# Kernel tuning notes

Hardware: AMD Instinct MI355X
Metric: run time of the kernel (lower is better)

Reference implementation:

```python
import jax, jax.numpy as jnp
import numpy as np

# Explicit-duration HSMM forward DP in log space.
# Recursion (all quantities in log space):
#   entry[t, j] = pi[j]                                   if t == 0
#               = logsumexp_i alpha[t-1, i] + A[i, j]      otherwise
#   alpha[t, j] = logsumexp_{d=1..min(Dmax, t+1)}
#                   entry[t-d+1, j] + D[j, d] + sum_{u=t-d+1..t} log_B[u, j]
#   loglik      = logsumexp_j alpha[T-1, j]

NEG = -1.0e30  # finite -inf sentinel (autodiff-safe)
B, T, S, DMAX = 64, 2048, 128, 128


def setup_inputs() -> dict:
    key = jax.random.key(0)
    k1, k2, k3, k4 = jax.random.split(key, 4)
    # emission log-likelihoods per (batch, time, state); need not normalize over states
    log_B = jax.random.normal(k1, (B, T, S), dtype=jnp.float32)
    # normalized log-prob buffers, matching the module's buffer constraints
    pi_logits = jax.nn.log_softmax(jax.random.normal(k2, (S,), dtype=jnp.float32))
    A_raw = jax.random.normal(k3, (S, S), dtype=jnp.float32)
    # SEMI transition constraint: no self-transitions (diagonal ~ -inf), rows normalized
    A_logits = jax.nn.log_softmax(
        jnp.where(jnp.eye(S, dtype=bool), -1.0e9, A_raw), axis=1)
    D_logits = jax.nn.log_softmax(
        jax.random.normal(k4, (S, DMAX), dtype=jnp.float32), axis=1)
    return {"log_B": log_B, "pi_logits": pi_logits,
            "A_logits": A_logits, "D_logits": D_logits}


def _hsmm_forward_loglik(log_B, pi_logits, A_logits, D_logits):
    Bn, Tn, Sn = log_B.shape
    Dm = D_logits.shape[1]
    lb = jnp.transpose(log_B, (1, 0, 2))                         # (T, B, S)
    # cum[k] = sum_{u < k} log_B[u]; front-padded with Dm zero rows (masked anyway)
    cum = jnp.concatenate(
        [jnp.zeros((1, Bn, Sn), lb.dtype), jnp.cumsum(lb, axis=0)], axis=0)
    cum_pad = jnp.concatenate(
        [jnp.zeros((Dm, Bn, Sn), lb.dtype), cum], axis=0)        # (T+Dm+1, B, S)
    logD = D_logits.T[:, None, :]                                # (Dm, 1, S)
    dur = jnp.arange(1, Dm + 1)[:, None, None]                   # (Dm, 1, 1)

    def step(carry, t):
        entry_buf, alpha_prev = carry                            # (Dm,B,S), (B,S)
        # transition into state j after a segment ended at t-1
        trans = jax.nn.logsumexp(
            alpha_prev[:, :, None] + A_logits[None, :, :], axis=1)  # (B, S)
        entry_t = jnp.where(t == 0, pi_logits[None, :], trans)
        # entry_buf[d-1] = entry[t-d+1]
        entry_buf = jnp.roll(entry_buf, 1, axis=0).at[0].set(entry_t)
        # segment emission sums: seg[d-1] = cum[t+1] - cum[t+1-d]
        win = jax.lax.dynamic_slice_in_dim(cum_pad, t + 1, Dm, axis=0)
        end = jax.lax.dynamic_slice_in_dim(cum_pad, t + Dm + 1, 1, axis=0)
        seg = end - jnp.flip(win, axis=0)                        # (Dm, B, S)
        scores = entry_buf + logD + seg
        scores = jnp.where(dur <= t + 1, scores, NEG)            # mask d > t+1
        alpha_t = jax.nn.logsumexp(scores, axis=0)               # (B, S)
        return (entry_buf, alpha_t), None

    init = (jnp.full((Dm, Bn, Sn), NEG, lb.dtype),
            jnp.full((Bn, Sn), NEG, lb.dtype))
    (_, alpha_last), _ = jax.lax.scan(step, init, jnp.arange(Tn))
    return jax.nn.logsumexp(alpha_last, axis=1)                  # (B,)


def reference(log_B, pi_logits, A_logits, D_logits):
    return _hsmm_forward_loglik(log_B, pi_logits, A_logits, D_logits)
```

## Files before the change

### kernel.cpp

```cpp
#include <hip/hip_runtime.h>

#define TT 2048
#define SS 128
#define DMAXX 128
#define NBATCH 64

typedef float f2 __attribute__((ext_vector_type(2)));

__device__ __forceinline__ float fexp2(float x){ return __builtin_amdgcn_exp2f(x); }
__device__ __forceinline__ float flog2(float x){ return __builtin_amdgcn_logf(x); }
__device__ __forceinline__ float frcp (float x){ return __builtin_amdgcn_rcpf(x); }
__device__ __forceinline__ f2 pkfma(f2 a, f2 b, f2 c){ return __builtin_elementwise_fma(a, b, c); }

template<int CTRL>
__device__ __forceinline__ float dppf(float x) {
    int i = __float_as_int(x);
    return __int_as_float(__builtin_amdgcn_update_dpp(i, i, CTRL, 0xF, 0xF, false));
}
#define DPP_XOR1   0xB1
#define DPP_XOR2   0x4E
#define DPP_SHUP1  0x90
#define DPP_ROR4   0x124
#define DPP_ROR8   0x128
#define DPP_BC15   0x142
#define DPP_BC31   0x143

constexpr float LOG2E = 1.4426950408889634f;
constexpr float LN2   = 0.6931471805599453f;

struct State {
    f2    rp[16];
    f2    eAp[16];
    f2    eDp[32];
    float eD0;
    float pf[4];
    const float* pfp;
    float C2;
    float e_pi;
    float G;
    float dsP;
};

struct Ctx {
    const float4* up0; const float4* up1;
    const f2*     wmp;
    float* uaw0; float* uaw1;
    float* wmwp;
    bool q0, l63;
};

template<int PHI>
__device__ __forceinline__ void hsmm_step(State& st, const Ctx& c, int tb)
{
    constexpr int  rho    = 31 - PHI;
    constexpr int  rhoN   = 31 - ((PHI + 1) & 31);
    constexpr int  pb     = (PHI + 1) & 1;
    constexpr int  wb     = PHI & 1;
    constexpr bool DO_WM  = ((PHI & 7) == 6);
    constexpr bool DO_RN  = ((PHI & 7) == 7);
    constexpr bool REBASE = (PHI == 31);
    const int t = tb + PHI;

    const float4* up = pb ? c.up1 : c.up0;
    float4 v[8];
#pragma unroll
    for (int k = 0; k < 8; ++k) v[k] = up[k];

    float xB = st.pf[PHI & 3];
    if (t + 4 < TT) st.pf[PHI & 3] = st.pfp[0];
    st.pfp += SS;
    float g = fexp2(xB * LOG2E);
    if constexpr (DO_RN) {
        f2 wv = *c.wmp;
        float m = fmaxf(wv.x, wv.y);
        m = fmaxf(m, dppf<DPP_XOR1>(m));
        m = fmaxf(m, dppf<DPP_XOR2>(m));
        st.C2 += flog2(m);
        g *= frcp(m);
    }
    float rG = frcp(st.G);
    float Gn = st.G * g;
    st.G = Gn;

    f2 a0, a1, a2, a3;
    {
        f2 u;
        u = (f2){v[0].x, v[0].y}; a0 = u * st.eAp[0];
        u = (f2){v[0].z, v[0].w}; a1 = u * st.eAp[1];
        u = (f2){v[1].x, v[1].y}; a2 = u * st.eAp[2];
        u = (f2){v[1].z, v[1].w}; a3 = u * st.eAp[3];
#pragma unroll
        for (int kk = 2; kk < 8; kk += 2) {
            u = (f2){v[kk].x,     v[kk].y};     a0 = pkfma(u, st.eAp[2 * kk],     a0);
            u = (f2){v[kk].z,     v[kk].w};     a1 = pkfma(u, st.eAp[2 * kk + 1], a1);
            u = (f2){v[kk + 1].x, v[kk + 1].y}; a2 = pkfma(u, st.eAp[2 * kk + 2], a2);
            u = (f2){v[kk + 1].z, v[kk + 1].w}; a3 = pkfma(u, st.eAp[2 * kk + 3], a3);
        }
    }
    f2 asum = (a0 + a1) + (a2 + a3);
    float tp = asum.x + asum.y;
    tp += dppf<DPP_XOR1>(tp);
    tp += dppf<DPP_XOR2>(tp);
    if constexpr (PHI == 0) { if (tb == 0) tp = st.e_pi; }

    float U = fmaf(tp * g, st.eD0, st.dsP * Gn);
    if (c.q0) {
        float fr = tp * rG;
        if constexpr (rho & 1) st.rp[rho >> 1].y = fr;
        else                   st.rp[rho >> 1].x = fr;
        *(wb ? c.uaw1 : c.uaw0) = U;
    }

    if constexpr (DO_WM) {
        float wm = U;
        wm = fmaxf(wm, dppf<DPP_ROR4>(wm));
        wm = fmaxf(wm, dppf<DPP_ROR8>(wm));
        wm = fmaxf(wm, dppf<DPP_BC15>(wm));
        wm = fmaxf(wm, dppf<DPP_BC31>(wm));
        if (c.l63) *c.wmwp = wm;
    }

    if constexpr (REBASE) {
        f2 GG = {Gn, Gn};
#pragma unroll
        for (int m2 = 0; m2 < 16; ++m2) st.rp[m2] = st.rp[m2] * GG;
        st.G = 1.f;
    }

    float rold;
    if constexpr (rhoN & 1) rold = st.rp[rhoN >> 1].y; else rold = st.rp[rhoN >> 1].x;
    float car = dppf<DPP_SHUP1>(rold);
    float ins = c.q0 ? 0.f : car;
    if constexpr (rhoN & 1) st.rp[rhoN >> 1].y = ins;
    else                    st.rp[rhoN >> 1].x = ins;

    f2 q0a = {0.f, 0.f}, q1a = {0.f, 0.f}, q2a = {0.f, 0.f}, q3a = {0.f, 0.f};
#pragma unroll
    for (int m2 = 0; m2 < 16; m2 += 4) {
        q0a = pkfma(st.rp[m2],     st.eDp[(2 * m2 + PHI + 2) & 31], q0a);
        q1a = pkfma(st.rp[m2 + 1], st.eDp[(2 * m2 + PHI + 4) & 31], q1a);
        q2a = pkfma(st.rp[m2 + 2], st.eDp[(2 * m2 + PHI + 6) & 31], q2a);
        q3a = pkfma(st.rp[m2 + 3], st.eDp[(2 * m2 + PHI + 8) & 31], q3a);
    }
    f2 qs = (q0a + q1a) + (q2a + q3a);
    float ds = qs.x + qs.y;
    ds += dppf<DPP_XOR1>(ds);
    ds += dppf<DPP_XOR2>(ds);
    st.dsP = ds;

    asm volatile("s_waitcnt lgkmcnt(0)\n\ts_barrier" ::: "memory");
}

__launch_bounds__(512, 2)
__global__ void hsmm_fwd_kernel(const float* __restrict__ logB,
                                const float* __restrict__ pi,
                                const float* __restrict__ A,
                                const float* __restrict__ D,
                                float* __restrict__ out)
{
    const int b   = blockIdx.x;
    const int tid = threadIdx.x;
    const int l   = tid & 63;
    const int w   = tid >> 6;
    const int j   = tid >> 2;
    const int q   = tid & 3;

    __shared__ __align__(16) float ua[2][4 * 36];
    __shared__ __align__(16) float wmaxf[8];

    State st;
#pragma unroll
    for (int k = 0; k < 16; ++k) {
        st.eAp[k].x = fexp2(A[(q * 32 + 2 * k)     * SS + j] * LOG2E);
        st.eAp[k].y = fexp2(A[(q * 32 + 2 * k + 1) * SS + j] * LOG2E);
    }
    {
        float eD[32];
#pragma unroll
        for (int k = 0; k < 32; ++k)
            eD[k] = fexp2(D[j * DMAXX + q * 32 + k] * LOG2E);
#pragma unroll
        for (int wdx = 0; wdx < 32; ++wdx) {
            st.eDp[wdx].x = eD[wdx];
            st.eDp[wdx].y = eD[(wdx + 1) & 31];
        }
    }
#pragma unroll
    for (int k = 0; k < 16; ++k) st.rp[k] = (f2){0.f, 0.f};
    st.eD0  = fexp2(D[j * DMAXX] * LOG2E);
    st.C2   = 0.f;
    st.e_pi = fexp2(pi[j] * LOG2E);
    st.G    = 1.f;
    st.dsP  = 0.f;

    const float* __restrict__ lb = logB + ((size_t)b * TT) * SS + j;
#pragma unroll
    for (int k = 0; k < 4; ++k) st.pf[k] = lb[(size_t)k * SS];
    st.pfp = lb + (size_t)4 * SS;

    Ctx c;
    c.up0  = (const float4*)&ua[0][q * 36];
    c.up1  = (const float4*)&ua[1][q * 36];
    c.wmp  = (const f2*)&wmaxf[2 * q];
    c.q0   = (q == 0);
    c.l63  = (l == 63);
    c.uaw0 = &ua[0][(j >> 5) * 36 + (j & 31)];
    c.uaw1 = &ua[1][(j >> 5) * 36 + (j & 31)];
    c.wmwp = &wmaxf[w];

    for (int tb = 0; tb < TT; tb += 32) {
        hsmm_step< 0>(st, c, tb); hsmm_step< 1>(st, c, tb);
        hsmm_step< 2>(st, c, tb); hsmm_step< 3>(st, c, tb);
        hsmm_step< 4>(st, c, tb); hsmm_step< 5>(st, c, tb);
        hsmm_step< 6>(st, c, tb); hsmm_step< 7>(st, c, tb);
        hsmm_step< 8>(st, c, tb); hsmm_step< 9>(st, c, tb);
        hsmm_step<10>(st, c, tb); hsmm_step<11>(st, c, tb);
        hsmm_step<12>(st, c, tb); hsmm_step<13>(st, c, tb);
        hsmm_step<14>(st, c, tb); hsmm_step<15>(st, c, tb);
        hsmm_step<16>(st, c, tb); hsmm_step<17>(st, c, tb);
        hsmm_step<18>(st, c, tb); hsmm_step<19>(st, c, tb);
        hsmm_step<20>(st, c, tb); hsmm_step<21>(st, c, tb);
        hsmm_step<22>(st, c, tb); hsmm_step<23>(st, c, tb);
        hsmm_step<24>(st, c, tb); hsmm_step<25>(st, c, tb);
        hsmm_step<26>(st, c, tb); hsmm_step<27>(st, c, tb);
        hsmm_step<28>(st, c, tb); hsmm_step<29>(st, c, tb);
        hsmm_step<30>(st, c, tb); hsmm_step<31>(st, c, tb);
    }

    if (tid == 0) {
        float s = 0.f;
        for (int i = 0; i < SS; ++i) s += ua[1][(i >> 5) * 36 + (i & 31)];
        out[b] = (st.C2 + flog2(s)) * LN2;
    }
}

extern "C" void kernel_launch(void* const* d_in, const int* in_sizes, int n_in,
                              void* d_out, int out_size, void* d_ws, size_t ws_size,
                              hipStream_t stream) {
    const float* logB = (const float*)d_in[0];
    const float* pi   = (const float*)d_in[1];
    const float* A    = (const float*)d_in[2];
    const float* D    = (const float*)d_in[3];
    float* out        = (float*)d_out;
    hipLaunchKernelGGL(hsmm_fwd_kernel, dim3(NBATCH), dim3(512), 0, stream,
                       logB, pi, A, D, out);
}
```

Before: 830.8 us.

## Remap threads so each lane reads two float4 of alpha and transposes reduction

Changes the thread-to-(state, quarter) mapping so each lane holds A entries for 4 destination states over an 8-source slice. The per-step LDS read drops from eight float4 to two, and the transition sum uses a transpose-style DPP reduction across lanes. The duration carry shift now uses a row-shift DPP with bound control that zero-fills, which removes a select. The LDS layout and the max-reduction patterns are adjusted to match, at the cost of extra selects and DPP ops in the reduction.

```diff
diff --git a/kernel.cpp b/kernel.cpp
--- a/kernel.cpp
+++ b/kernel.cpp
@@ -17,9 +17,14 @@
     int i = __float_as_int(x);
     return __int_as_float(__builtin_amdgcn_update_dpp(i, i, CTRL, 0xF, 0xF, false));
 }
+template<int CTRL>
+__device__ __forceinline__ float dppzf(float x) {
+    int i = __float_as_int(x);
+    return __int_as_float(__builtin_amdgcn_update_dpp(0, i, CTRL, 0xF, 0xF, true));
+}
 #define DPP_XOR1   0xB1
 #define DPP_XOR2   0x4E
-#define DPP_SHUP1  0x90
+#define DPP_RSHR4  0x114
 #define DPP_ROR4   0x124
 #define DPP_ROR8   0x128
 #define DPP_BC15   0x142
@@ -30,7 +35,7 @@
 
 struct State {
     f2    rp[16];
-    f2    eAp[16];
+    f2    eApk[16];
     f2    eDp[32];
     float eD0;
     float pf[4];
@@ -46,7 +51,7 @@
     const f2*     wmp;
     float* uaw0; float* uaw1;
     float* wmwp;
-    bool q0, l63;
+    bool q0, l63, b0, b1;
 };
 
 template<int PHI>
@@ -62,9 +67,8 @@
     const int t = tb + PHI;
 
     const float4* up = pb ? c.up1 : c.up0;
-    float4 v[8];
-#pragma unroll
-    for (int k = 0; k < 8; ++k) v[k] = up[k];
+    float4 va = up[0];
+    float4 vb = up[1];
 
     float xB = st.pf[PHI & 3];
     if (t + 4 < TT) st.pf[PHI & 3] = st.pfp[0];
@@ -82,25 +86,31 @@
     float Gn = st.G * g;
     st.G = Gn;
 
-    f2 a0, a1, a2, a3;
-    {
-        f2 u;
-        u = (f2){v[0].x, v[0].y}; a0 = u * st.eAp[0];
-        u = (f2){v[0].z, v[0].w}; a1 = u * st.eAp[1];
-        u = (f2){v[1].x, v[1].y}; a2 = u * st.eAp[2];
-        u = (f2){v[1].z, v[1].w}; a3 = u * st.eAp[3];
-#pragma unroll
-        for (int kk = 2; kk < 8; kk += 2) {
-            u = (f2){v[kk].x,     v[kk].y};     a0 = pkfma(u, st.eAp[2 * kk],     a0);
-            u = (f2){v[kk].z,     v[kk].w};     a1 = pkfma(u, st.eAp[2 * kk + 1], a1);
-            u = (f2){v[kk + 1].x, v[kk + 1].y}; a2 = pkfma(u, st.eAp[2 * kk + 2], a2);
-            u = (f2){v[kk + 1].z, v[kk + 1].w}; a3 = pkfma(u, st.eAp[2 * kk + 3], a3);
-        }
-    }
-    f2 asum = (a0 + a1) + (a2 + a3);
-    float tp = asum.x + asum.y;
-    tp += dppf<DPP_XOR1>(tp);
-    tp += dppf<DPP_XOR2>(tp);
+    f2 a0, a1, a2, a3, u;
+    u = (f2){va.x, va.y};
+    a0 = u * st.eApk[0];  a1 = u * st.eApk[4];  a2 = u * st.eApk[8];  a3 = u * st.eApk[12];
+    u = (f2){va.z, va.w};
+    a0 = pkfma(u, st.eApk[1], a0); a1 = pkfma(u, st.eApk[5], a1);
+    a2 = pkfma(u, st.eApk[9], a2); a3 = pkfma(u, st.eApk[13], a3);
+    u = (f2){vb.x, vb.y};
+    a0 = pkfma(u, st.eApk[2], a0); a1 = pkfma(u, st.eApk[6], a1);
+    a2 = pkfma(u, st.eApk[10], a2); a3 = pkfma(u, st.eApk[14], a3);
+    u = (f2){vb.z, vb.w};
+    a0 = pkfma(u, st.eApk[3], a0); a1 = pkfma(u, st.eApk[7], a1);
+    a2 = pkfma(u, st.eApk[11], a2); a3 = pkfma(u, st.eApk[15], a3);
+
+    float h0 = a0.x + a0.y, h1 = a1.x + a1.y, h2 = a2.x + a2.y, h3 = a3.x + a3.y;
+    float s1 = c.b0 ? h0 : h1;
+    float k1 = c.b0 ? h1 : h0;
+    float m01 = k1 + dppf<DPP_XOR1>(s1);
+    float s2 = c.b0 ? h2 : h3;
+    float k2 = c.b0 ? h3 : h2;
+    float m23 = k2 + dppf<DPP_XOR1>(s2);
+    float s3 = c.b1 ? m01 : m23;
+    float k3 = c.b1 ? m23 : m01;
+    float tp = k3 + dppf<DPP_XOR2>(s3);
+    tp += dppf<DPP_ROR4>(tp);
+    tp += dppf<DPP_ROR8>(tp);
     if constexpr (PHI == 0) { if (tb == 0) tp = st.e_pi; }
 
     float U = fmaf(tp * g, st.eD0, st.dsP * Gn);
@@ -113,8 +123,8 @@
 
     if constexpr (DO_WM) {
         float wm = U;
-        wm = fmaxf(wm, dppf<DPP_ROR4>(wm));
-        wm = fmaxf(wm, dppf<DPP_ROR8>(wm));
+        wm = fmaxf(wm, dppf<DPP_XOR1>(wm));
+        wm = fmaxf(wm, dppf<DPP_XOR2>(wm));
         wm = fmaxf(wm, dppf<DPP_BC15>(wm));
         wm = fmaxf(wm, dppf<DPP_BC31>(wm));
         if (c.l63) *c.wmwp = wm;
@@ -129,8 +139,7 @@
 
     float rold;
     if constexpr (rhoN & 1) rold = st.rp[rhoN >> 1].y; else rold = st.rp[rhoN >> 1].x;
-    float car = dppf<DPP_SHUP1>(rold);
-    float ins = c.q0 ? 0.f : car;
+    float ins = dppzf<DPP_RSHR4>(rold);
     if constexpr (rhoN & 1) st.rp[rhoN >> 1].y = ins;
     else                    st.rp[rhoN >> 1].x = ins;
 
@@ -144,8 +153,8 @@
     }
     f2 qs = (q0a + q1a) + (q2a + q3a);
     float ds = qs.x + qs.y;
-    ds += dppf<DPP_XOR1>(ds);
-    ds += dppf<DPP_XOR2>(ds);
+    ds += dppf<DPP_ROR4>(ds);
+    ds += dppf<DPP_ROR8>(ds);
     st.dsP = ds;
 
     asm volatile("s_waitcnt lgkmcnt(0)\n\ts_barrier" ::: "memory");
@@ -158,22 +167,28 @@
                                 const float* __restrict__ D,
                                 float* __restrict__ out)
 {
-    const int b   = blockIdx.x;
-    const int tid = threadIdx.x;
-    const int l   = tid & 63;
-    const int w   = tid >> 6;
-    const int j   = tid >> 2;
-    const int q   = tid & 3;
-
-    __shared__ __align__(16) float ua[2][4 * 36];
+    const int b    = blockIdx.x;
+    const int tid  = threadIdx.x;
+    const int l    = tid & 63;
+    const int w    = tid >> 6;
+    const int r    = (l >> 4);
+    const int sIdx = l & 15;
+    const int cc   = l & 3;
+    const int q    = (l >> 2) & 3;
+    const int j4   = w * 16 + r * 4;
+    const int j    = j4 + cc;
+
+    __shared__ __align__(16) float ua[2][16 * 12];
     __shared__ __align__(16) float wmaxf[8];
 
     State st;
 #pragma unroll
-    for (int k = 0; k < 16; ++k) {
-        st.eAp[k].x = fexp2(A[(q * 32 + 2 * k)     * SS + j] * LOG2E);
-        st.eAp[k].y = fexp2(A[(q * 32 + 2 * k + 1) * SS + j] * LOG2E);
-    }
+    for (int cp = 0; cp < 4; ++cp)
+#pragma unroll
+        for (int m = 0; m < 4; ++m) {
+            st.eApk[cp * 4 + m].x = fexp2(A[(8 * sIdx + 2 * m)     * SS + j4 + cp] * LOG2E);
+            st.eApk[cp * 4 + m].y = fexp2(A[(8 * sIdx + 2 * m + 1) * SS + j4 + cp] * LOG2E);
+        }
     {
         float eD[32];
 #pragma unroll
@@ -199,13 +214,15 @@
     st.pfp = lb + (size_t)4 * SS;
 
     Ctx c;
-    c.up0  = (const float4*)&ua[0][q * 36];
-    c.up1  = (const float4*)&ua[1][q * 36];
-    c.wmp  = (const f2*)&wmaxf[2 * q];
+    c.up0  = (const float4*)&ua[0][sIdx * 12];
+    c.up1  = (const float4*)&ua[1][sIdx * 12];
+    c.wmp  = (const f2*)&wmaxf[2 * cc];
     c.q0   = (q == 0);
     c.l63  = (l == 63);
-    c.uaw0 = &ua[0][(j >> 5) * 36 + (j & 31)];
-    c.uaw1 = &ua[1][(j >> 5) * 36 + (j & 31)];
+    c.b0   = (l & 1);
+    c.b1   = ((l & 2) != 0);
+    c.uaw0 = &ua[0][(j >> 3) * 12 + (j & 7)];
+    c.uaw1 = &ua[1][(j >> 3) * 12 + (j & 7)];
     c.wmwp = &wmaxf[w];
 
     for (int tb = 0; tb < TT; tb += 32) {
@@ -229,7 +246,7 @@
 
     if (tid == 0) {
         float s = 0.f;
-        for (int i = 0; i < SS; ++i) s += ua[1][(i >> 5) * 36 + (i & 31)];
+        for (int i = 0; i < SS; ++i) s += ua[1][(i >> 3) * 12 + (i & 7)];
         out[b] = (st.C2 + flog2(s)) * LN2;
     }
 }
```

Measured after the change: 842.0 us. About the same (+1.4%).
